# Performance work log

Measured on AMD Instinct MI355X. Metric: run time of the kernel, lower is better.

The kernel has to match this reference:

```python
import jax, jax.numpy as jnp
import numpy as np
import math

N, J = 8192, 22  # N = batch*frames (per-frame calls are independent), J = num_joint


def _layernorm(x, g, b, eps=1e-5):
    m = jnp.mean(x, axis=-1, keepdims=True)
    v = jnp.var(x, axis=-1, keepdims=True)
    return (x - m) * jax.lax.rsqrt(v + eps) * g + b


def _attention(x, Wqkv, bqkv, Wo, bo, heads):
    # x: [B, n, d]; matches torch Attention (scale = d**-0.5)
    B, n, d = x.shape
    hd = d // heads
    qkv = (x @ Wqkv + bqkv).reshape(B, n, 3, heads, hd).transpose(2, 0, 3, 1, 4)
    q, k, v = qkv[0], qkv[1], qkv[2]  # [B, h, n, hd]
    dots = jnp.einsum('bhid,bhjd->bhij', q, k) * (d ** -0.5)
    attn = jax.nn.softmax(dots, axis=-1)
    out = jnp.einsum('bhij,bhjd->bhid', attn, v)
    out = out.transpose(0, 2, 1, 3).reshape(B, n, -1)
    return out @ Wo + bo


def _encoder(x, tok_W, tok_b, qkv_W, qkv_b, o_W, o_b, ln_g, ln_b, m1_W, m1_b, m2_W, m2_b, heads):
    tok = x @ tok_W + tok_b                                   # [B, J, 64]
    h = _attention(tok, qkv_W, qkv_b, o_W, o_b, heads)        # [B, J, out_dim]
    hn = _layernorm(h, ln_g, ln_b)
    mlp = jax.nn.relu(hn @ m1_W + m1_b) @ m2_W + m2_b
    return h + mlp                                            # Residual(LN+MLP)


def _sinusoidal_pe(max_len, dim):
    pos = np.arange(max_len)[:, None].astype(np.float32)
    div = np.exp(np.arange(0, dim, 2, dtype=np.float32) * (-math.log(10000.0) / dim))
    pe = np.zeros((max_len, dim), dtype=np.float32)
    pe[:, 0::2] = np.sin(pos * div)
    pe[:, 1::2] = np.cos(pos * div)
    return jnp.asarray(pe)


def setup_inputs() -> dict:
    key = jax.random.key(0)
    ks = iter(jax.random.split(key, 64))
    rn = lambda shape, s=0.1: jax.random.normal(next(ks), shape, dtype=jnp.float32) * s
    inp = {
        'q_t': jax.random.normal(next(ks), (N, J, 4), dtype=jnp.float32),
        'skelA': jax.random.normal(next(ks), (N, J, 3), dtype=jnp.float32),
        'skelB': jax.random.normal(next(ks), (N, J, 3), dtype=jnp.float32),
        'quat_mean': jax.random.normal(next(ks), (J, 4), dtype=jnp.float32) * 0.1,
        'quat_std': jax.random.uniform(next(ks), (J, 4), dtype=jnp.float32, minval=0.5, maxval=1.5),
        # QuatEncoder params
        'qe_tok_W': rn((4, 64)), 'qe_tok_b': jnp.zeros((64,), jnp.float32),
        'qe_qkv_W': rn((64, 192)), 'qe_qkv_b': jnp.zeros((192,), jnp.float32),
        'qe_o_W': rn((64, 256)), 'qe_o_b': jnp.zeros((256,), jnp.float32),
        'qe_ln_g': jnp.ones((256,), jnp.float32), 'qe_ln_b': jnp.zeros((256,), jnp.float32),
        'qe_m1_W': rn((256, 512)), 'qe_m1_b': jnp.zeros((512,), jnp.float32),
        'qe_m2_W': rn((512, 256)), 'qe_m2_b': jnp.zeros((256,), jnp.float32),
        # shared SeklEncoder params
        'se_tok_W': rn((3, 64)), 'se_tok_b': jnp.zeros((64,), jnp.float32),
        'se_qkv_W': rn((64, 192)), 'se_qkv_b': jnp.zeros((192,), jnp.float32),
        'se_o_W': rn((64, 128)), 'se_o_b': jnp.zeros((128,), jnp.float32),
        'se_ln_g': jnp.ones((128,), jnp.float32), 'se_ln_b': jnp.zeros((128,), jnp.float32),
        'se_m1_W': rn((128, 256)), 'se_m1_b': jnp.zeros((256,), jnp.float32),
        'se_m2_W': rn((256, 128)), 'se_m2_b': jnp.zeros((128,), jnp.float32),
        # head
        'emb_W': rn((512, 128)), 'emb_b': jnp.zeros((128,), jnp.float32),
        'del_W': rn((128, 4)), 'del_b': jnp.zeros((4,), jnp.float32),
    }
    return inp


def reference(q_t, skelA, skelB, quat_mean, quat_std,
              qe_tok_W, qe_tok_b, qe_qkv_W, qe_qkv_b, qe_o_W, qe_o_b,
              qe_ln_g, qe_ln_b, qe_m1_W, qe_m1_b, qe_m2_W, qe_m2_b,
              se_tok_W, se_tok_b, se_qkv_W, se_qkv_b, se_o_W, se_o_b,
              se_ln_g, se_ln_b, se_m1_W, se_m1_b, se_m2_W, se_m2_b,
              emb_W, emb_b, del_W, del_b):
    q_embed = _encoder(q_t, qe_tok_W, qe_tok_b, qe_qkv_W, qe_qkv_b, qe_o_W, qe_o_b,
                       qe_ln_g, qe_ln_b, qe_m1_W, qe_m1_b, qe_m2_W, qe_m2_b, heads=4)   # [N,J,256]
    sA = _encoder(skelA, se_tok_W, se_tok_b, se_qkv_W, se_qkv_b, se_o_W, se_o_b,
                  se_ln_g, se_ln_b, se_m1_W, se_m1_b, se_m2_W, se_m2_b, heads=2)        # [N,J,128]
    sB = _encoder(skelB, se_tok_W, se_tok_b, se_qkv_W, se_qkv_b, se_o_W, se_o_b,
                  se_ln_g, se_ln_b, se_m1_W, se_m1_b, se_m2_W, se_m2_b, heads=2)        # [N,J,128]
    cat = jnp.concatenate([q_embed, sA, sB], axis=-1)                                   # [N,J,512]
    dim = cat.shape[-1]
    pe = _sinusoidal_pe(J, dim)
    pos = cat * math.sqrt(dim) + pe[None, :, :]
    embed = jax.nn.relu(pos @ emb_W + emb_b)                                            # [N,J,128]
    delta = embed @ del_W + del_b                                                       # [N,J,4]
    delta = delta * quat_std + quat_mean
    # normalized()
    lengths = jnp.sqrt(jnp.sum(delta * delta, axis=-1, keepdims=True))
    return delta / lengths
```

## Files before the change

### kernel.cpp

```cpp
#include <hip/hip_runtime.h>
#include <hip/hip_bf16.h>
#include <math.h>

#define NJ 22
#define MROWS 44
#define PROWS 48
#define NRT 3

typedef float f4 __attribute__((ext_vector_type(4)));
typedef _Float16 h8 __attribute__((ext_vector_type(8)));

#define WOFF_QE_QKV 0
#define WOFF_QE_O   24576
#define WOFF_QE_M1  57344
#define WOFF_QE_M2  319488
#define WOFF_SE_QKV 581632
#define WOFF_SE_O   606208
#define WOFF_SE_M1  622592
#define WOFF_SE_M2  688128
#define WOFF_EMB    753664

struct Smem {
    _Float16 XH[PROWS * 256];
    __align__(16) char U[PROWS * 128 * 4];
    float LNp[PROWS * 4], LNq[PROWS * 4];
    float LNm[PROWS], LNr[PROWS];
    float Sx[MROWS * 4];
    float Sd[MROWS * 4];
};

struct Args {
    const float *q_t, *skelA, *skelB, *quat_mean, *quat_std;
    const float *qe_tok_W, *qe_tok_b, *qe_qkv_b, *qe_o_b, *qe_ln_g, *qe_ln_b, *qe_m1_b, *qe_m2_b;
    const float *se_tok_W, *se_tok_b, *se_qkv_b, *se_o_b, *se_ln_g, *se_ln_b, *se_m1_b, *se_m2_b;
    const float *del_W, *del_b;
    const float *P;
    const _Float16 *W;
    float *out;
};

__device__ __forceinline__ int swz(int r, int c) {
    return (((c >> 3) ^ (r & 7)) << 3) | (c & 7);
}

template<int NI, int KSTEPS, int LDA>
__device__ __forceinline__ void mfma_gemm(f4 (&acc)[NI][NRT],
        const _Float16 *AH,
        const _Float16 *BH, const _Float16 *BL,
        int wK, int koff, int w, int l) {
    const int m = l & 15, q = l >> 4;
#pragma unroll 1
    for (int s = 0; s < KSTEPS; s++) {
        const int ka = s * 32 + q * 8;
        h8 a[NRT];
#pragma unroll
        for (int rt = 0; rt < NRT; rt++) {
            int r = rt * 16 + m;
            a[rt] = *(const h8 *)(AH + r * LDA + (((ka >> 3) ^ (r & 7)) << 3));
        }
#pragma unroll
        for (int i = 0; i < NI; i++) {
            int n = (w + 4 * i) * 16 + m;
            int boff = n * wK + koff + ka;
            h8 bh = *(const h8 *)(BH + boff);
            h8 bl = *(const h8 *)(BL + boff);
#pragma unroll
            for (int rt = 0; rt < NRT; rt++) {
                acc[i][rt] = __builtin_amdgcn_mfma_f32_16x16x32_f16(a[rt], bh, acc[i][rt], 0, 0, 0);
                acc[i][rt] = __builtin_amdgcn_mfma_f32_16x16x32_f16(a[rt], bl, acc[i][rt], 0, 0, 0);
            }
        }
    }
}

template<int NH, int HD>
__device__ __forceinline__ void attention(Smem &sm, int t) {
    constexpr int SPL = HD / 16;
    if (t < NH * MROWS * SPL) {
        const int half = t & (SPL - 1);
        const int ur = t / SPL;
        const int hh = ur / MROWS;
        const int rr = ur - hh * MROWS;
        const int jb = (rr >= NJ) ? NJ : 0;
        const float *KF = (const float *)sm.U;
        const float *VF = KF + PROWS * 64;
        const int c0 = 64 + hh * HD + half * 16;
        float qv[16];
#pragma unroll
        for (int g = 0; g < 2; g++) {
            h8 qh = *(const h8 *)(sm.XH + rr * 256 + swz(rr, c0 + g * 8));
#pragma unroll
            for (int d = 0; d < 8; d++) qv[g * 8 + d] = (float)qh[d];
        }
        float s[NJ];
        float mx = -1e30f;
#pragma unroll
        for (int j = 0; j < NJ; j++) {
            const float *kp = KF + (jb + j) * 64 + hh * HD + half * 16;
            float acc = 0.f;
#pragma unroll
            for (int d = 0; d < 16; d += 4) {
                float4 v = *(const float4 *)(kp + d);
                acc += qv[d] * v.x + qv[d + 1] * v.y + qv[d + 2] * v.z + qv[d + 3] * v.w;
            }
            if constexpr (SPL == 2) acc += __shfl_xor(acc, 1);
            s[j] = acc * 0.125f;
            mx = fmaxf(mx, s[j]);
        }
        float sum = 0.f;
#pragma unroll
        for (int j = 0; j < NJ; j++) { s[j] = __expf(s[j] - mx); sum += s[j]; }
        float inv = 1.f / sum;
        float o[16];
#pragma unroll
        for (int d = 0; d < 16; d++) o[d] = 0.f;
#pragma unroll
        for (int j = 0; j < NJ; j++) {
            float p = s[j] * inv;
            const float *vp = VF + (jb + j) * 64 + hh * HD + half * 16;
#pragma unroll
            for (int d = 0; d < 16; d += 4) {
                float4 v = *(const float4 *)(vp + d);
                o[d] = fmaf(p, v.x, o[d]);       o[d + 1] = fmaf(p, v.y, o[d + 1]);
                o[d + 2] = fmaf(p, v.z, o[d + 2]); o[d + 3] = fmaf(p, v.w, o[d + 3]);
            }
        }
        const int cw = hh * HD + half * 16;
#pragma unroll
        for (int g = 0; g < 2; g++) {
            h8 oh;
#pragma unroll
            for (int d = 0; d < 8; d++) oh[d] = (_Float16)o[g * 8 + d];
            *(h8 *)(sm.XH + rr * 256 + swz(rr, cw + g * 8)) = oh;
        }
    }
}

template<int D, int NH, int TK>
__device__ __forceinline__ void encode(Smem &sm, const float *__restrict__ xg,
        const float *__restrict__ tokW, const float *__restrict__ tokB,
        const float *__restrict__ qkvB, const float *__restrict__ oB,
        const float *__restrict__ lnG,  const float *__restrict__ lnB,
        const float *__restrict__ m1B,  const float *__restrict__ m2B,
        const _Float16 *__restrict__ Wq,  const _Float16 *__restrict__ Wo,
        const _Float16 *__restrict__ Wm1, const _Float16 *__restrict__ Wm2,
        const _Float16 *__restrict__ Wemb, int embKoff,
        f4 (&emb)[2][NRT], int t, int w, int l) {
    constexpr int NI = D / 64;
    constexpr int HID = 2 * D;
    const int m = l & 15, q = l >> 4;

    if (t < MROWS * TK) sm.Sx[t] = xg[t];
    __syncthreads();
    {
        float b = tokB[l];
#pragma unroll
        for (int i = 0; i < 11; i++) {
            int r = w + 4 * i;
            float acc = b;
#pragma unroll
            for (int k = 0; k < TK; k++)
                acc = fmaf(sm.Sx[r * TK + k], tokW[k * 64 + l], acc);
            sm.XH[r * 256 + swz(r, l)] = (_Float16)acc;
        }
    }
    __syncthreads();
    {
        f4 acc[3][NRT];
#pragma unroll
        for (int i = 0; i < 3; i++)
#pragma unroll
            for (int rt = 0; rt < NRT; rt++) acc[i][rt] = (f4){0.f, 0.f, 0.f, 0.f};
        mfma_gemm<3, 2, 256>(acc, sm.XH, Wq, Wq + 192 * 64, 64, 0, w, l);
        float *KV = (float *)sm.U;
#pragma unroll
        for (int i = 0; i < 3; i++) {
            int c = (w + 4 * i) * 16 + m;
            float b = qkvB[c];
#pragma unroll
            for (int rt = 0; rt < NRT; rt++)
#pragma unroll
                for (int e = 0; e < 4; e++) {
                    int r = rt * 16 + q * 4 + e;
                    float v = acc[i][rt][e] + b;
                    sm.XH[r * 256 + swz(r, 64 + c)] = (_Float16)v;
                    if (c >= 128)      KV[PROWS * 64 + r * 64 + (c - 128)] = v;
                    else if (c >= 64)  KV[r * 64 + (c - 64)] = v;
                }
        }
    }
    __syncthreads();
    attention<NH, 64 / NH>(sm, t);
    __syncthreads();
    f4 res[NI][NRT];
#pragma unroll
    for (int i = 0; i < NI; i++)
#pragma unroll
        for (int rt = 0; rt < NRT; rt++) res[i][rt] = (f4){0.f, 0.f, 0.f, 0.f};
    mfma_gemm<NI, 2, 256>(res, sm.XH, Wo, Wo + D * 64, 64, 0, w, l);
#pragma unroll
    for (int i = 0; i < NI; i++) {
        float b = oB[(w + 4 * i) * 16 + m];
#pragma unroll
        for (int rt = 0; rt < NRT; rt++)
#pragma unroll
            for (int e = 0; e < 4; e++) res[i][rt][e] += b;
    }
#pragma unroll
    for (int rt = 0; rt < NRT; rt++)
#pragma unroll
        for (int e = 0; e < 4; e++) {
            int r = rt * 16 + q * 4 + e;
            float s1 = 0.f, s2 = 0.f;
#pragma unroll
            for (int i = 0; i < NI; i++) {
                float v = res[i][rt][e];
                s1 += v; s2 = fmaf(v, v, s2);
            }
#pragma unroll
            for (int off = 8; off > 0; off >>= 1) {
                s1 += __shfl_xor(s1, off);
                s2 += __shfl_xor(s2, off);
            }
            if (m == 0) { sm.LNp[r * 4 + w] = s1; sm.LNq[r * 4 + w] = s2; }
        }
    __syncthreads();
    if (t < PROWS) {
        float s1 = sm.LNp[t * 4] + sm.LNp[t * 4 + 1] + sm.LNp[t * 4 + 2] + sm.LNp[t * 4 + 3];
        float s2 = sm.LNq[t * 4] + sm.LNq[t * 4 + 1] + sm.LNq[t * 4 + 2] + sm.LNq[t * 4 + 3];
        float mean = s1 * (1.f / D);
        float var = s2 * (1.f / D) - mean * mean;
        sm.LNm[t] = mean;
        sm.LNr[t] = rsqrtf(fmaxf(var, 0.f) + 1e-5f);
    }
    __syncthreads();
#pragma unroll
    for (int i = 0; i < NI; i++) {
        int c = (w + 4 * i) * 16 + m;
        float g = lnG[c], bb = lnB[c];
#pragma unroll
        for (int rt = 0; rt < NRT; rt++)
#pragma unroll
            for (int e = 0; e < 4; e++) {
                int r = rt * 16 + q * 4 + e;
                float v = (res[i][rt][e] - sm.LNm[r]) * sm.LNr[r] * g + bb;
                sm.XH[r * 256 + swz(r, c)] = (_Float16)v;
            }
    }
    __syncthreads();
    _Float16 *HH = (_Float16 *)sm.U;
#pragma unroll 1
    for (int cb = 0; cb < HID / 128; cb++) {
        f4 h1[2][NRT];
#pragma unroll
        for (int i = 0; i < 2; i++)
#pragma unroll
            for (int rt = 0; rt < NRT; rt++) h1[i][rt] = (f4){0.f, 0.f, 0.f, 0.f};
        mfma_gemm<2, D / 32, 256>(h1, sm.XH,
                                  Wm1 + cb * 128 * D, Wm1 + HID * D + cb * 128 * D, D, 0, w, l);
        __syncthreads();
#pragma unroll
        for (int i = 0; i < 2; i++) {
            int c = (w + 4 * i) * 16 + m;
            float b = m1B[cb * 128 + c];
#pragma unroll
            for (int rt = 0; rt < NRT; rt++)
#pragma unroll
                for (int e = 0; e < 4; e++) {
                    int r = rt * 16 + q * 4 + e;
                    HH[r * 128 + swz(r, c)] = (_Float16)fmaxf(h1[i][rt][e] + b, 0.f);
                }
        }
        __syncthreads();
        mfma_gemm<NI, 4, 128>(res, HH, Wm2, Wm2 + D * HID, HID, cb * 128, w, l);
    }
    __syncthreads();
#pragma unroll
    for (int i = 0; i < NI; i++) {
        int c = (w + 4 * i) * 16 + m;
        float b = m2B[c];
#pragma unroll
        for (int rt = 0; rt < NRT; rt++)
#pragma unroll
            for (int e = 0; e < 4; e++) {
                int r = rt * 16 + q * 4 + e;
                sm.XH[r * 256 + swz(r, c)] = (_Float16)(res[i][rt][e] + b);
            }
    }
    __syncthreads();
    mfma_gemm<2, D / 32, 256>(emb, sm.XH, Wemb, Wemb + 128 * 512, 512, embKoff, w, l);
}

__global__ __launch_bounds__(256, 2) void fused_kernel(Args A) {
    __shared__ __align__(16) Smem sm;
    const int t = threadIdx.x, w = t >> 6, l = t & 63;
    const int m = l & 15, q = l >> 4;
    const int blk = blockIdx.x;

    for (int i = t; i < 4 * 256; i += 256) {
        int r = MROWS + (i >> 8), c = i & 255;
        sm.XH[r * 256 + c] = (_Float16)0.f;
    }

    f4 emb[2][NRT];
#pragma unroll
    for (int i = 0; i < 2; i++)
#pragma unroll
        for (int rt = 0; rt < NRT; rt++) emb[i][rt] = (f4){0.f, 0.f, 0.f, 0.f};

    const _Float16 *W = A.W;
    const _Float16 *Wemb = W + WOFF_EMB;

    encode<256, 4, 4>(sm, A.q_t + blk * MROWS * 4,
                      A.qe_tok_W, A.qe_tok_b, A.qe_qkv_b, A.qe_o_b,
                      A.qe_ln_g, A.qe_ln_b, A.qe_m1_b, A.qe_m2_b,
                      W + WOFF_QE_QKV, W + WOFF_QE_O, W + WOFF_QE_M1, W + WOFF_QE_M2,
                      Wemb, 0, emb, t, w, l);
    encode<128, 2, 3>(sm, A.skelA + blk * MROWS * 3,
                      A.se_tok_W, A.se_tok_b, A.se_qkv_b, A.se_o_b,
                      A.se_ln_g, A.se_ln_b, A.se_m1_b, A.se_m2_b,
                      W + WOFF_SE_QKV, W + WOFF_SE_O, W + WOFF_SE_M1, W + WOFF_SE_M2,
                      Wemb, 256, emb, t, w, l);
    encode<128, 2, 3>(sm, A.skelB + blk * MROWS * 3,
                      A.se_tok_W, A.se_tok_b, A.se_qkv_b, A.se_o_b,
                      A.se_ln_g, A.se_ln_b, A.se_m1_b, A.se_m2_b,
                      W + WOFF_SE_QKV, W + WOFF_SE_O, W + WOFF_SE_M1, W + WOFF_SE_M2,
                      Wemb, 384, emb, t, w, l);

    __syncthreads();
    float *E = (float *)sm.U;
#pragma unroll
    for (int i = 0; i < 2; i++) {
        int c = (w + 4 * i) * 16 + m;
#pragma unroll
        for (int rt = 0; rt < NRT; rt++)
#pragma unroll
            for (int e = 0; e < 4; e++) {
                int r = rt * 16 + q * 4 + e;
                int j = (r >= NJ) ? r - NJ : r;
                j = (j >= NJ) ? 0 : j;
                float v = fmaf(22.627416997969522f, emb[i][rt][e], A.P[j * 128 + c]);
                E[r * 128 + c] = fmaxf(v, 0.f);
            }
    }
    __syncthreads();
    if (t < MROWS * 4) {
        int r = t >> 2, d = t & 3;
        float acc = A.del_b[d];
        for (int c = 0; c < 128; c++)
            acc = fmaf(E[r * 128 + c], A.del_W[c * 4 + d], acc);
        int j = (r >= NJ) ? r - NJ : r;
        acc = fmaf(acc, A.quat_std[j * 4 + d], A.quat_mean[j * 4 + d]);
        sm.Sd[t] = acc;
    }
    __syncthreads();
    if (t < MROWS * 4) {
        int r = t >> 2;
        float x0 = sm.Sd[r * 4], x1 = sm.Sd[r * 4 + 1];
        float x2 = sm.Sd[r * 4 + 2], x3 = sm.Sd[r * 4 + 3];
        float inv = 1.f / sqrtf(x0 * x0 + x1 * x1 + x2 * x2 + x3 * x3);
        A.out[blk * MROWS * 4 + t] = sm.Sd[t] * inv;
    }
}

struct WDesc { const float *W; int K; int N; int off; };
struct SplitArgs { WDesc d[9]; _Float16 *out; };

__global__ void split_kernel(SplitArgs a) {
    WDesc d = a.d[blockIdx.y];
    int e = blockIdx.x * 256 + threadIdx.x;
    int tot = d.K * d.N;
    if (e < tot) {
        int n = e / d.K, k = e - n * d.K;
        float v = d.W[k * d.N + n];
        _Float16 h = (_Float16)v;
        a.out[d.off + e] = h;
        a.out[d.off + tot + e] = (_Float16)(v - (float)h);
    }
}

__global__ void pe_emb_kernel(const float *__restrict__ emb_W,
                              const float *__restrict__ emb_b, float *P) {
    int r = blockIdx.x;
    int c = threadIdx.x;
    float acc = emb_b[c];
    const float k = -2.f * logf(10000.f) / 512.f;
    for (int i = 0; i < 256; i++) {
        float ang = (float)r * expf((float)i * k);
        acc = fmaf(sinf(ang), emb_W[(2 * i) * 128 + c], acc);
        acc = fmaf(cosf(ang), emb_W[(2 * i + 1) * 128 + c], acc);
    }
    P[r * 128 + c] = acc;
}

extern "C" void kernel_launch(void *const *d_in, const int *in_sizes, int n_in,
                              void *d_out, int out_size, void *d_ws, size_t ws_size,
                              hipStream_t stream) {
    const float **in = (const float **)d_in;
    float *P = (float *)d_ws;
    _Float16 *W = (_Float16 *)((float *)d_ws + 22 * 128);

    Args A;
    A.q_t = in[0]; A.skelA = in[1]; A.skelB = in[2]; A.quat_mean = in[3]; A.quat_std = in[4];
    A.qe_tok_W = in[5]; A.qe_tok_b = in[6]; A.qe_qkv_b = in[8]; A.qe_o_b = in[10];
    A.qe_ln_g = in[11]; A.qe_ln_b = in[12]; A.qe_m1_b = in[14]; A.qe_m2_b = in[16];
    A.se_tok_W = in[17]; A.se_tok_b = in[18]; A.se_qkv_b = in[20]; A.se_o_b = in[22];
    A.se_ln_g = in[23]; A.se_ln_b = in[24]; A.se_m1_b = in[26]; A.se_m2_b = in[28];
    A.del_W = in[31]; A.del_b = in[32];
    A.P = P; A.W = W; A.out = (float *)d_out;

    SplitArgs sa;
    sa.d[0] = { in[7],  64, 192, WOFF_QE_QKV };
    sa.d[1] = { in[9],  64, 256, WOFF_QE_O };
    sa.d[2] = { in[13], 256, 512, WOFF_QE_M1 };
    sa.d[3] = { in[15], 512, 256, WOFF_QE_M2 };
    sa.d[4] = { in[19], 64, 192, WOFF_SE_QKV };
    sa.d[5] = { in[21], 64, 128, WOFF_SE_O };
    sa.d[6] = { in[25], 128, 256, WOFF_SE_M1 };
    sa.d[7] = { in[27], 256, 128, WOFF_SE_M2 };
    sa.d[8] = { in[29], 512, 128, WOFF_EMB };
    sa.out = W;

    int n_items = in_sizes[0] / (NJ * 4);
    int blocks = n_items / 2;

    split_kernel<<<dim3(512, 9), 256, 0, stream>>>(sa);
    pe_emb_kernel<<<NJ, 128, 0, stream>>>(in[29], in[30], P);
    fused_kernel<<<blocks, 256, 0, stream>>>(A);
}
```

Baseline: 1.365 ms.

## Double block size to eight waves, splitting GEMM column tiles across more warps

Raises the fused kernel from 256 to 512 threads per block (8 waves), so each wave owns half as many 16-column output tiles in every MFMA GEMM. The QKV GEMM gets a guarded tail for its 12 tiles, and the LayerNorm partial sums grow to 8 per row. The goal is more latency hiding and less register pressure per wave for the same shared memory per block. Launch bounds now ask for 4 blocks of 512 threads. The risks are idle waves on uneven tile counts, more barrier cost across 8 waves, and each wave reloading the A fragments.

Result: slower. 1.573 ms (+15.2%).

```diff
diff --git a/kernel.cpp b/kernel.cpp
--- a/kernel.cpp
+++ b/kernel.cpp
@@ -6,6 +6,7 @@
 #define MROWS 44
 #define PROWS 48
 #define NRT 3
+#define NTHR 512
 
 typedef float f4 __attribute__((ext_vector_type(4)));
 typedef _Float16 h8 __attribute__((ext_vector_type(8)));
@@ -23,7 +24,7 @@
 struct Smem {
     _Float16 XH[PROWS * 256];
     __align__(16) char U[PROWS * 128 * 4];
-    float LNp[PROWS * 4], LNq[PROWS * 4];
+    float LNp[PROWS * 8], LNq[PROWS * 8];
     float LNm[PROWS], LNr[PROWS];
     float Sx[MROWS * 4];
     float Sd[MROWS * 4];
@@ -43,11 +44,12 @@
     return (((c >> 3) ^ (r & 7)) << 3) | (c & 7);
 }
 
-template<int NI, int KSTEPS, int LDA>
-__device__ __forceinline__ void mfma_gemm(f4 (&acc)[NI][NRT],
+template<int NT, int KSTEPS, int LDA>
+__device__ __forceinline__ void mfma_gemm(f4 (&acc)[(NT + 7) / 8][NRT],
         const _Float16 *AH,
         const _Float16 *BH, const _Float16 *BL,
         int wK, int koff, int w, int l) {
+    constexpr int NI = (NT + 7) / 8;
     const int m = l & 15, q = l >> 4;
 #pragma unroll 1
     for (int s = 0; s < KSTEPS; s++) {
@@ -60,14 +62,16 @@
         }
 #pragma unroll
         for (int i = 0; i < NI; i++) {
-            int n = (w + 4 * i) * 16 + m;
-            int boff = n * wK + koff + ka;
-            h8 bh = *(const h8 *)(BH + boff);
-            h8 bl = *(const h8 *)(BL + boff);
-#pragma unroll
-            for (int rt = 0; rt < NRT; rt++) {
-                acc[i][rt] = __builtin_amdgcn_mfma_f32_16x16x32_f16(a[rt], bh, acc[i][rt], 0, 0, 0);
-                acc[i][rt] = __builtin_amdgcn_mfma_f32_16x16x32_f16(a[rt], bl, acc[i][rt], 0, 0, 0);
+            if (NT % 8 == 0 || w + 8 * i < NT) {
+                int n = (w + 8 * i) * 16 + m;
+                int boff = n * wK + koff + ka;
+                h8 bh = *(const h8 *)(BH + boff);
+                h8 bl = *(const h8 *)(BL + boff);
+#pragma unroll
+                for (int rt = 0; rt < NRT; rt++) {
+                    acc[i][rt] = __builtin_amdgcn_mfma_f32_16x16x32_f16(a[rt], bh, acc[i][rt], 0, 0, 0);
+                    acc[i][rt] = __builtin_amdgcn_mfma_f32_16x16x32_f16(a[rt], bl, acc[i][rt], 0, 0, 0);
+                }
             }
         }
     }
@@ -145,48 +149,53 @@
         const _Float16 *__restrict__ Wq,  const _Float16 *__restrict__ Wo,
         const _Float16 *__restrict__ Wm1, const _Float16 *__restrict__ Wm2,
         const _Float16 *__restrict__ Wemb, int embKoff,
-        f4 (&emb)[2][NRT], int t, int w, int l) {
-    constexpr int NI = D / 64;
+        f4 (&emb)[1][NRT], int t, int w, int l) {
+    constexpr int NI = D / 128;
     constexpr int HID = 2 * D;
     const int m = l & 15, q = l >> 4;
 
     if (t < MROWS * TK) sm.Sx[t] = xg[t];
     __syncthreads();
+    if (l < 64) {
+        float b = tokB[l];
+#pragma unroll
+        for (int i = 0; i < 6; i++) {
+            int r = w + 8 * i;
+            if (r < MROWS) {
+                float acc = b;
+#pragma unroll
+                for (int k = 0; k < TK; k++)
+                    acc = fmaf(sm.Sx[r * TK + k], tokW[k * 64 + l], acc);
+                sm.XH[r * 256 + swz(r, l)] = (_Float16)acc;
+            }
+        }
+    }
+    __syncthreads();
     {
-        float b = tokB[l];
-#pragma unroll
-        for (int i = 0; i < 11; i++) {
-            int r = w + 4 * i;
-            float acc = b;
-#pragma unroll
-            for (int k = 0; k < TK; k++)
-                acc = fmaf(sm.Sx[r * TK + k], tokW[k * 64 + l], acc);
-            sm.XH[r * 256 + swz(r, l)] = (_Float16)acc;
-        }
-    }
-    __syncthreads();
-    {
-        f4 acc[3][NRT];
-#pragma unroll
-        for (int i = 0; i < 3; i++)
+        f4 acc[2][NRT];
+#pragma unroll
+        for (int i = 0; i < 2; i++)
 #pragma unroll
             for (int rt = 0; rt < NRT; rt++) acc[i][rt] = (f4){0.f, 0.f, 0.f, 0.f};
-        mfma_gemm<3, 2, 256>(acc, sm.XH, Wq, Wq + 192 * 64, 64, 0, w, l);
+        mfma_gemm<12, 2, 256>(acc, sm.XH, Wq, Wq + 192 * 64, 64, 0, w, l);
         float *KV = (float *)sm.U;
 #pragma unroll
-        for (int i = 0; i < 3; i++) {
-            int c = (w + 4 * i) * 16 + m;
-            float b = qkvB[c];
-#pragma unroll
-            for (int rt = 0; rt < NRT; rt++)
-#pragma unroll
-                for (int e = 0; e < 4; e++) {
-                    int r = rt * 16 + q * 4 + e;
-                    float v = acc[i][rt][e] + b;
-                    sm.XH[r * 256 + swz(r, 64 + c)] = (_Float16)v;
-                    if (c >= 128)      KV[PROWS * 64 + r * 64 + (c - 128)] = v;
-                    else if (c >= 64)  KV[r * 64 + (c - 64)] = v;
-                }
+        for (int i = 0; i < 2; i++) {
+            int tile = w + 8 * i;
+            if (tile < 12) {
+                int c = tile * 16 + m;
+                float b = qkvB[c];
+#pragma unroll
+                for (int rt = 0; rt < NRT; rt++)
+#pragma unroll
+                    for (int e = 0; e < 4; e++) {
+                        int r = rt * 16 + q * 4 + e;
+                        float v = acc[i][rt][e] + b;
+                        sm.XH[r * 256 + swz(r, 64 + c)] = (_Float16)v;
+                        if (c >= 128)      KV[PROWS * 64 + r * 64 + (c - 128)] = v;
+                        else if (c >= 64)  KV[r * 64 + (c - 64)] = v;
+                    }
+            }
         }
     }
     __syncthreads();
@@ -197,10 +206,10 @@
     for (int i = 0; i < NI; i++)
 #pragma unroll
         for (int rt = 0; rt < NRT; rt++) res[i][rt] = (f4){0.f, 0.f, 0.f, 0.f};
-    mfma_gemm<NI, 2, 256>(res, sm.XH, Wo, Wo + D * 64, 64, 0, w, l);
+    mfma_gemm<D / 16, 2, 256>(res, sm.XH, Wo, Wo + D * 64, 64, 0, w, l);
 #pragma unroll
     for (int i = 0; i < NI; i++) {
-        float b = oB[(w + 4 * i) * 16 + m];
+        float b = oB[(w + 8 * i) * 16 + m];
 #pragma unroll
         for (int rt = 0; rt < NRT; rt++)
 #pragma unroll
@@ -222,12 +231,13 @@
                 s1 += __shfl_xor(s1, off);
                 s2 += __shfl_xor(s2, off);
             }
-            if (m == 0) { sm.LNp[r * 4 + w] = s1; sm.LNq[r * 4 + w] = s2; }
+            if (m == 0) { sm.LNp[r * 8 + w] = s1; sm.LNq[r * 8 + w] = s2; }
         }
     __syncthreads();
     if (t < PROWS) {
-        float s1 = sm.LNp[t * 4] + sm.LNp[t * 4 + 1] + sm.LNp[t * 4 + 2] + sm.LNp[t * 4 + 3];
-        float s2 = sm.LNq[t * 4] + sm.LNq[t * 4 + 1] + sm.LNq[t * 4 + 2] + sm.LNq[t * 4 + 3];
+        float s1 = 0.f, s2 = 0.f;
+#pragma unroll
+        for (int k2 = 0; k2 < 8; k2++) { s1 += sm.LNp[t * 8 + k2]; s2 += sm.LNq[t * 8 + k2]; }
         float mean = s1 * (1.f / D);
         float var = s2 * (1.f / D) - mean * mean;
         sm.LNm[t] = mean;
@@ -236,7 +246,7 @@
     __syncthreads();
 #pragma unroll
     for (int i = 0; i < NI; i++) {
-        int c = (w + 4 * i) * 16 + m;
+        int c = (w + 8 * i) * 16 + m;
         float g = lnG[c], bb = lnB[c];
 #pragma unroll
         for (int rt = 0; rt < NRT; rt++)
@@ -251,33 +261,30 @@
     _Float16 *HH = (_Float16 *)sm.U;
 #pragma unroll 1
     for (int cb = 0; cb < HID / 128; cb++) {
-        f4 h1[2][NRT];
-#pragma unroll
-        for (int i = 0; i < 2; i++)
-#pragma unroll
-            for (int rt = 0; rt < NRT; rt++) h1[i][rt] = (f4){0.f, 0.f, 0.f, 0.f};
-        mfma_gemm<2, D / 32, 256>(h1, sm.XH,
+        f4 h1[1][NRT];
+#pragma unroll
+        for (int rt = 0; rt < NRT; rt++) h1[0][rt] = (f4){0.f, 0.f, 0.f, 0.f};
+        mfma_gemm<8, D / 32, 256>(h1, sm.XH,
                                   Wm1 + cb * 128 * D, Wm1 + HID * D + cb * 128 * D, D, 0, w, l);
         __syncthreads();
-#pragma unroll
-        for (int i = 0; i < 2; i++) {
-            int c = (w + 4 * i) * 16 + m;
+        {
+            int c = w * 16 + m;
             float b = m1B[cb * 128 + c];
 #pragma unroll
             for (int rt = 0; rt < NRT; rt++)
 #pragma unroll
                 for (int e = 0; e < 4; e++) {
                     int r = rt * 16 + q * 4 + e;
-                    HH[r * 128 + swz(r, c)] = (_Float16)fmaxf(h1[i][rt][e] + b, 0.f);
+                    HH[r * 128 + swz(r, c)] = (_Float16)fmaxf(h1[0][rt][e] + b, 0.f);
                 }
         }
         __syncthreads();
-        mfma_gemm<NI, 4, 128>(res, HH, Wm2, Wm2 + D * HID, HID, cb * 128, w, l);
+        mfma_gemm<D / 16, 4, 128>(res, HH, Wm2, Wm2 + D * HID, HID, cb * 128, w, l);
     }
     __syncthreads();
 #pragma unroll
     for (int i = 0; i < NI; i++) {
-        int c = (w + 4 * i) * 16 + m;
+        int c = (w + 8 * i) * 16 + m;
         float b = m2B[c];
 #pragma unroll
         for (int rt = 0; rt < NRT; rt++)
@@ -288,25 +295,23 @@
             }
     }
     __syncthreads();
-    mfma_gemm<2, D / 32, 256>(emb, sm.XH, Wemb, Wemb + 128 * 512, 512, embKoff, w, l);
-}
-
-__global__ __launch_bounds__(256, 2) void fused_kernel(Args A) {
+    mfma_gemm<8, D / 32, 256>(emb, sm.XH, Wemb, Wemb + 128 * 512, 512, embKoff, w, l);
+}
+
+__global__ __launch_bounds__(NTHR, 4) void fused_kernel(Args A) {
     __shared__ __align__(16) Smem sm;
     const int t = threadIdx.x, w = t >> 6, l = t & 63;
     const int m = l & 15, q = l >> 4;
     const int blk = blockIdx.x;
 
-    for (int i = t; i < 4 * 256; i += 256) {
+    for (int i = t; i < 4 * 256; i += NTHR) {
         int r = MROWS + (i >> 8), c = i & 255;
         sm.XH[r * 256 + c] = (_Float16)0.f;
     }
 
-    f4 emb[2][NRT];
-#pragma unroll
-    for (int i = 0; i < 2; i++)
-#pragma unroll
-        for (int rt = 0; rt < NRT; rt++) emb[i][rt] = (f4){0.f, 0.f, 0.f, 0.f};
+    f4 emb[1][NRT];
+#pragma unroll
+    for (int rt = 0; rt < NRT; rt++) emb[0][rt] = (f4){0.f, 0.f, 0.f, 0.f};
 
     const _Float16 *W = A.W;
     const _Float16 *Wemb = W + WOFF_EMB;
@@ -329,9 +334,8 @@
 
     __syncthreads();
     float *E = (float *)sm.U;
-#pragma unroll
-    for (int i = 0; i < 2; i++) {
-        int c = (w + 4 * i) * 16 + m;
+    {
+        int c = w * 16 + m;
 #pragma unroll
         for (int rt = 0; rt < NRT; rt++)
 #pragma unroll
@@ -339,7 +343,7 @@
                 int r = rt * 16 + q * 4 + e;
                 int j = (r >= NJ) ? r - NJ : r;
                 j = (j >= NJ) ? 0 : j;
-                float v = fmaf(22.627416997969522f, emb[i][rt][e], A.P[j * 128 + c]);
+                float v = fmaf(22.627416997969522f, emb[0][rt][e], A.P[j * 128 + c]);
                 E[r * 128 + c] = fmaxf(v, 0.f);
             }
     }
@@ -426,5 +430,5 @@
 
     split_kernel<<<dim3(512, 9), 256, 0, stream>>>(sa);
     pe_emb_kernel<<<NJ, 128, 0, stream>>>(in[29], in[30], P);
-    fused_kernel<<<blocks, 256, 0, stream>>>(A);
-}
+    fused_kernel<<<blocks, NTHR, 0, stream>>>(A);
+}
```
